# Performance work log

Hardware: AMD Instinct MI355X
Metric: run time of the kernel (lower is better)

Reference implementation:

```python
import jax, jax.numpy as jnp
import numpy as np

B, TQ, TK, D, H = 8, 1024, 1024, 1024, 16
HD = D // H
EPS = 1e-5


def layernorm(x, g, b):
    mu = jnp.mean(x, axis=-1, keepdims=True)
    var = jnp.mean(jnp.square(x - mu), axis=-1, keepdims=True)
    return (x - mu) * jax.lax.rsqrt(var + EPS) * g + b


def setup_inputs() -> dict:
    key = jax.random.key(0)
    ks = jax.random.split(key, 16)
    s = 1.0 / np.sqrt(D)
    return {
        "base": jax.random.normal(ks[0], (B, TQ, D), jnp.float32),
        "fusion": jax.random.normal(ks[1], (B, TK, D), jnp.float32),
        "Wq": jax.random.normal(ks[2], (D, D), jnp.float32) * s,
        "Wk": jax.random.normal(ks[3], (D, D), jnp.float32) * s,
        "Wv": jax.random.normal(ks[4], (D, D), jnp.float32) * s,
        "Wo": jax.random.normal(ks[5], (D, D), jnp.float32) * s,
        "g1": jnp.ones((D,), jnp.float32),
        "b1": jnp.zeros((D,), jnp.float32),
        "g2": jnp.ones((D,), jnp.float32),
        "b2": jnp.zeros((D,), jnp.float32),
        "fc1_w": jax.random.normal(ks[6], (D, D), jnp.float32) * s,
        "fc1_b": jnp.zeros((D,), jnp.float32),
        "fc2_w": jax.random.normal(ks[7], (D, D), jnp.float32) * s,
        "fc2_b": jnp.zeros((D,), jnp.float32),
        "rw": jax.random.normal(ks[8], (D, D), jnp.float32) * s,
        "rb": jnp.zeros((D,), jnp.float32),
        "alpha": jnp.asarray(0.1, jnp.float32),
    }


def reference(base, fusion, Wq, Wk, Wv, Wo, g1, b1, g2, b2,
              fc1_w, fc1_b, fc2_w, fc2_b, rw, rb, alpha):
    def split_heads(x):  # [B,T,D] -> [B,H,T,hd]
        return x.reshape(B, -1, H, HD).transpose(0, 2, 1, 3)

    Q = split_heads(base @ Wq.T)
    K = split_heads(fusion @ Wk.T)
    V = split_heads(fusion @ Wv.T)

    scores = jnp.einsum("bhqd,bhkd->bhqk", Q, K) / jnp.sqrt(jnp.float32(HD))
    attn = jax.nn.softmax(scores, axis=-1)
    # threshold mask (the torch scatter_ with arange indices is an identity copy)
    masked = attn * (attn >= alpha).astype(attn.dtype)
    # second softmax over masked weights (zeros contribute exp(0)=1, as in the original)
    attn2 = jax.nn.softmax(masked, axis=-1)
    out = jnp.einsum("bhqk,bhkd->bhqd", attn2, V)
    out = out.transpose(0, 2, 1, 3).reshape(B, TQ, D)
    out = out @ Wo.T
    x = layernorm(base + out, g1, b1)  # dropout is eval-mode identity
    ff = jax.nn.silu(jax.nn.silu(x @ fc1_w.T + fc1_b) @ fc2_w.T + fc2_b)
    y = layernorm(x + ff, g2, b2)
    final = y @ rw.T + rb
    return final, masked
```

## Files before the change

kernel.cpp:

```cpp
#include <hip/hip_runtime.h>


typedef unsigned short u16;
typedef __attribute__((ext_vector_type(8))) short  bf16x8;
typedef __attribute__((ext_vector_type(4))) short  s16x4;
typedef __attribute__((ext_vector_type(4))) float  f32x4;

#define GLL16(gp, lp) __builtin_amdgcn_global_load_lds(                     \
    (__attribute__((address_space(1))) const void*)(gp),                    \
    (__attribute__((address_space(3))) void*)(lp), 16, 0, 0)

__device__ __forceinline__ u16 f2bf(float x) {
  union { float f; unsigned u; } v; v.f = x;
  return (u16)((v.u + 0x7FFF + ((v.u >> 16) & 1)) >> 16);
}
__device__ __forceinline__ float bf2f(u16 h) {
  union { unsigned u; float f; } v; v.u = ((unsigned)h) << 16;
  return v.f;
}
__device__ __forceinline__ f32x4 zero4() { f32x4 z = {0.f, 0.f, 0.f, 0.f}; return z; }

__global__ __launch_bounds__(256) void pack_act(const float* __restrict__ a,
                                                const float* __restrict__ b,
                                                u16* __restrict__ outa,
                                                u16* __restrict__ outb) {
  size_t i = (size_t)blockIdx.x * 256 + threadIdx.x;
  const f32x4* in = (const f32x4*)(blockIdx.y ? b : a);
  s16x4* out = (s16x4*)(blockIdx.y ? outb : outa);
  f32x4 v = in[i];
  s16x4 o;
  o[0] = (short)f2bf(v[0]); o[1] = (short)f2bf(v[1]);
  o[2] = (short)f2bf(v[2]); o[3] = (short)f2bf(v[3]);
  out[i] = o;
}

__global__ __launch_bounds__(256) void pack_w(
    const float* __restrict__ w0, const float* __restrict__ w1,
    const float* __restrict__ w2, const float* __restrict__ w3,
    const float* __restrict__ w4, const float* __restrict__ w5,
    const float* __restrict__ w6, u16* __restrict__ out) {
  size_t i = (size_t)blockIdx.x * 256 + threadIdx.x;
  const float* in;
  switch (blockIdx.y) {
    case 0: in = w0; break;  case 1: in = w1; break;
    case 2: in = w2; break;  case 3: in = w3; break;
    case 4: in = w4; break;  case 5: in = w5; break;
    default: in = w6; break;
  }
  f32x4 v = ((const f32x4*)in)[i];
  s16x4 o;
  o[0] = (short)f2bf(v[0]); o[1] = (short)f2bf(v[1]);
  o[2] = (short)f2bf(v[2]); o[3] = (short)f2bf(v[3]);
  ((s16x4*)(out + (size_t)blockIdx.y * 1048576))[i] = o;
}

#define EPI_QKV       0
#define EPI_BF16      1
#define EPI_SILU_BF16 4
#define EPI_BIAS_F32  6

template <int EPI>
__global__ __launch_bounds__(256) void gemm_bt(
    const u16* __restrict__ A, int lda,
    const u16* __restrict__ W, int ldw,
    int M, int N, int K,
    float* __restrict__ outF, u16* __restrict__ outU,
    const float* __restrict__ bias,
    const u16* __restrict__ A2) {
  __shared__ u16 As[2][128 * 32];
  __shared__ u16 Bs[2][128 * 32];
  int tid = threadIdx.x;
  int l = tid & 63, w = tid >> 6;
  int wr = w >> 1, wc = w & 1, lr = l & 15, lq = l >> 4;

  int fid = blockIdx.y * 8 + blockIdx.x;
  int swz = (fid & 7) * 64 + (fid >> 3);
  int m0 = (swz >> 3) * 128, n0 = (swz & 7) * 128;

  const u16* Ap = A;
  const u16* Wp = W;
  u16* outUp = outU;
  if constexpr (EPI == EPI_QKV) {
    int z = blockIdx.z;
    if (z) Ap = A2;
    Wp = W + (size_t)z * 1048576;
    outUp = outU + (size_t)z * 8388608;
  }

  f32x4 acc[4][4];
#pragma unroll
  for (int i = 0; i < 4; i++)
#pragma unroll
    for (int j = 0; j < 4; j++) acc[i][j] = zero4();

  auto stage = [&](const u16* src, int ld, int r0, int k0, u16* lds) {
#pragma unroll
    for (int j = 0; j < 2; ++j) {
      int seg = j * 256 + tid;
      int row = seg >> 2, sp = seg & 3;
      const u16* g = src + (size_t)(r0 + row) * ld + k0 +
                     ((sp ^ ((row >> 1) & 3)) << 3);
      GLL16(g, lds + seg * 8);
    }
  };

  int nk = K >> 5;
  stage(Ap, lda, m0, 0, As[0]);
  stage(Wp, ldw, n0, 0, Bs[0]);
  for (int kt = 0; kt < nk; ++kt) {
    __syncthreads();
    if (kt + 1 < nk) {
      stage(Ap, lda, m0, (kt + 1) << 5, As[(kt + 1) & 1]);
      stage(Wp, ldw, n0, (kt + 1) << 5, Bs[(kt + 1) & 1]);
    }
    const u16* Ab = As[kt & 1];
    const u16* Bb = Bs[kt & 1];
    bf16x8 af[4], bw[4];
    int slot = (lq ^ ((lr >> 1) & 3)) << 3;
#pragma unroll
    for (int mi = 0; mi < 4; mi++)
      af[mi] = *(const bf16x8*)&Ab[(wr * 64 + mi * 16 + lr) * 32 + slot];
#pragma unroll
    for (int ni = 0; ni < 4; ni++)
      bw[ni] = *(const bf16x8*)&Bb[(wc * 64 + ni * 16 + lr) * 32 + slot];
#pragma unroll
    for (int mi = 0; mi < 4; mi++)
#pragma unroll
      for (int ni = 0; ni < 4; ni++)
        acc[mi][ni] = __builtin_amdgcn_mfma_f32_16x16x32_bf16(af[mi], bw[ni],
                                                              acc[mi][ni], 0, 0, 0);
  }

#pragma unroll
  for (int mi = 0; mi < 4; mi++) {
#pragma unroll
    for (int ni = 0; ni < 4; ni++) {
      int col = n0 + wc * 64 + ni * 16 + lr;
#pragma unroll
      for (int r = 0; r < 4; r++) {
        int row = m0 + wr * 64 + mi * 16 + lq * 4 + r;
        float v = acc[mi][ni][r];
        if constexpr (EPI == EPI_QKV) {
          int b = row >> 10, t = row & 1023, h = col >> 6, d = col & 63;
          int z = blockIdx.z;
          if (z == 0) {
            outUp[((size_t)(b * 16 + h) * 1024 + t) * 64 + d] = f2bf(v);
          } else if (z == 1) {
            size_t base = ((size_t)(b * 16 + h) * 1024 + t) * 64;
            outUp[base + (((d >> 3) ^ (t & 7)) << 3) + (d & 7)] = f2bf(v);
          } else {
            size_t o = ((size_t)(b * 16 + h) * 64 + d) * 1024 + (t & ~63) +
                       ((((t >> 3) & 7) ^ (d & 7)) << 3) + (t & 7);
            outUp[o] = f2bf(v);
          }
        } else if constexpr (EPI == EPI_BF16) {
          outUp[(size_t)row * N + col] = f2bf(v);
        } else if constexpr (EPI == EPI_SILU_BF16) {
          float z = v + bias[col];
          outUp[(size_t)row * N + col] = f2bf(z / (1.f + __expf(-z)));
        } else {
          outF[(size_t)row * N + col] = v + bias[col];
        }
      }
    }
  }
}

template <int EPI>
__global__ __launch_bounds__(512) void gemm_bt8(
    const u16* __restrict__ A, int lda,
    const u16* __restrict__ W, int ldw,
    int M, int N, int K,
    float* __restrict__ outF, u16* __restrict__ outU,
    const float* __restrict__ bias) {
  __shared__ u16 As[2][128 * 64];
  __shared__ u16 Bs[2][128 * 64];
  int tid = threadIdx.x;
  int l = tid & 63, w = tid >> 6;
  int wr = w >> 2, wc = w & 3, lr = l & 15, lq = l >> 4;

  int fid = blockIdx.y * 8 + blockIdx.x;
  int swz = (fid & 7) * 64 + (fid >> 3);
  int m0 = (swz >> 3) * 128, n0 = (swz & 7) * 128;

  f32x4 acc[4][2];
#pragma unroll
  for (int i = 0; i < 4; i++)
#pragma unroll
    for (int j = 0; j < 2; j++) acc[i][j] = zero4();

  auto stage = [&](const u16* src, int ld, int r0, int k0, u16* lds) {
#pragma unroll
    for (int j = 0; j < 2; ++j) {
      int seg = j * 512 + tid;
      int row = seg >> 3, sp = seg & 7;
      const u16* g = src + (size_t)(r0 + row) * ld + k0 +
                     ((sp ^ (row & 7)) << 3);
      GLL16(g, lds + seg * 8);
    }
  };

  int nk = K >> 6;
  stage(A, lda, m0, 0, As[0]);
  stage(W, ldw, n0, 0, Bs[0]);
  for (int kt = 0; kt < nk; ++kt) {
    __syncthreads();
    if (kt + 1 < nk) {
      stage(A, lda, m0, (kt + 1) << 6, As[(kt + 1) & 1]);
      stage(W, ldw, n0, (kt + 1) << 6, Bs[(kt + 1) & 1]);
    }
    const u16* Ab = As[kt & 1];
    const u16* Bb = Bs[kt & 1];
    bf16x8 af[4][2], bw[2][2];
#pragma unroll
    for (int kk = 0; kk < 2; kk++) {
      int slot = ((kk * 4 + lq) ^ (lr & 7)) << 3;
#pragma unroll
      for (int mi = 0; mi < 4; mi++)
        af[mi][kk] = *(const bf16x8*)&Ab[(wr * 64 + mi * 16 + lr) * 64 + slot];
#pragma unroll
      for (int ni = 0; ni < 2; ni++)
        bw[ni][kk] = *(const bf16x8*)&Bb[(wc * 32 + ni * 16 + lr) * 64 + slot];
    }
#pragma unroll
    for (int kk = 0; kk < 2; kk++)
#pragma unroll
      for (int mi = 0; mi < 4; mi++)
#pragma unroll
        for (int ni = 0; ni < 2; ni++)
          acc[mi][ni] = __builtin_amdgcn_mfma_f32_16x16x32_bf16(
              af[mi][kk], bw[ni][kk], acc[mi][ni], 0, 0, 0);
  }

#pragma unroll
  for (int mi = 0; mi < 4; mi++) {
#pragma unroll
    for (int ni = 0; ni < 2; ni++) {
      int col = n0 + wc * 32 + ni * 16 + lr;
#pragma unroll
      for (int r = 0; r < 4; r++) {
        int row = m0 + wr * 64 + mi * 16 + lq * 4 + r;
        float v = acc[mi][ni][r];
        if constexpr (EPI == EPI_BF16) {
          outU[(size_t)row * N + col] = f2bf(v);
        } else if constexpr (EPI == EPI_SILU_BF16) {
          float z = v + bias[col];
          outU[(size_t)row * N + col] = f2bf(z / (1.f + __expf(-z)));
        } else {
          outF[(size_t)row * N + col] = v + bias[col];
        }
      }
    }
  }
}

__global__ __launch_bounds__(512) void attn_kernel(
    const u16* __restrict__ Q2, const u16* __restrict__ K2,
    const u16* __restrict__ Vt, const float* __restrict__ alphap,
    float* __restrict__ masked_out, u16* __restrict__ attn_out) {
  __shared__ __align__(16) u16 Ks[2][4096];
  __shared__ __align__(16) u16 Vs[2][4096];
  __shared__ __align__(16) u16 Ps[8][16 * 72];

  int tid = threadIdx.x;
  int l = tid & 63, w = tid >> 6, lr = l & 15, lq = l >> 4;

  int bid = blockIdx.x;
  int qi  = bid >> 7;
  int bh  = (bid & 7) * 16 + ((bid >> 3) & 15);
  int h = bh & 15, b = bh >> 4;
  int q0 = qi * 128;

  const u16* Qb = Q2 + (size_t)bh * 1024 * 64;
  const u16* Kb = K2 + (size_t)bh * 1024 * 64;
  const u16* Vb = Vt + (size_t)bh * 64 * 1024;
  float alpha = alphap[0];
  int qw = q0 + w * 16;

  auto stageK = [&](int kc, u16* dst) {
    int seg = tid;
    GLL16(Kb + (size_t)kc * 4096 + seg * 8, dst + seg * 8);
  };
  auto stageV = [&](int kc, u16* dst) {
    int seg = tid;
    GLL16(Vb + (size_t)(seg >> 3) * 1024 + kc * 64 + (seg & 7) * 8, dst + seg * 8);
  };

  bf16x8 qf[2];
#pragma unroll
  for (int kt = 0; kt < 2; kt++)
    qf[kt] = *(const bf16x8*)(Qb + (size_t)(qw + lr) * 64 + kt * 32 + lq * 8);

  float s1[4] = {0.f, 0.f, 0.f, 0.f};

  stageK(0, Ks[0]);
  for (int kc = 0; kc < 16; ++kc) {
    __syncthreads();
    if (kc + 1 < 16) stageK(kc + 1, Ks[(kc + 1) & 1]);
    const u16* Kc = Ks[kc & 1];
    f32x4 acc[4];
#pragma unroll
    for (int ni = 0; ni < 4; ni++) acc[ni] = zero4();
    __builtin_amdgcn_s_setprio(1);
#pragma unroll
    for (int ni = 0; ni < 4; ++ni) {
      int t = ni * 16 + lr;
      bf16x8 k0 = *(const bf16x8*)&Kc[t * 64 + (((0 + lq) ^ (lr & 7)) << 3)];
      bf16x8 k1 = *(const bf16x8*)&Kc[t * 64 + (((4 + lq) ^ (lr & 7)) << 3)];
      acc[ni] = __builtin_amdgcn_mfma_f32_16x16x32_bf16(qf[0], k0, acc[ni], 0, 0, 0);
      acc[ni] = __builtin_amdgcn_mfma_f32_16x16x32_bf16(qf[1], k1, acc[ni], 0, 0, 0);
    }
    __builtin_amdgcn_s_setprio(0);
#pragma unroll
    for (int ni = 0; ni < 4; ni++)
#pragma unroll
      for (int r = 0; r < 4; r++)
        s1[r] += __expf(acc[ni][r] * 0.125f);
  }
#pragma unroll
  for (int r = 0; r < 4; r++) {
    float v = s1[r];
    v += __shfl_xor(v, 1); v += __shfl_xor(v, 2);
    v += __shfl_xor(v, 4); v += __shfl_xor(v, 8);
    s1[r] = 1.0f / v;
  }

  float s2[4] = {0.f, 0.f, 0.f, 0.f};
  f32x4 oacc[4];
#pragma unroll
  for (int dg = 0; dg < 4; dg++) oacc[dg] = zero4();

  stageK(0, Ks[0]);
  stageV(0, Vs[0]);
  for (int kc = 0; kc < 16; ++kc) {
    if (kc == 0) {
      asm volatile("s_waitcnt vmcnt(0) lgkmcnt(0)" ::: "memory");
    } else {
      asm volatile("s_waitcnt vmcnt(16) lgkmcnt(0)" ::: "memory");
    }
    __builtin_amdgcn_s_barrier();
    __builtin_amdgcn_sched_barrier(0);
    if (kc + 1 < 16) {
      stageK(kc + 1, Ks[(kc + 1) & 1]);
      stageV(kc + 1, Vs[(kc + 1) & 1]);
    }
    const u16* Kc = Ks[kc & 1];
    const u16* Vc = Vs[kc & 1];

    f32x4 acc[4];
#pragma unroll
    for (int ni = 0; ni < 4; ni++) acc[ni] = zero4();
    __builtin_amdgcn_s_setprio(1);
#pragma unroll
    for (int ni = 0; ni < 4; ++ni) {
      int t = ni * 16 + lr;
      bf16x8 k0 = *(const bf16x8*)&Kc[t * 64 + (((0 + lq) ^ (lr & 7)) << 3)];
      bf16x8 k1 = *(const bf16x8*)&Kc[t * 64 + (((4 + lq) ^ (lr & 7)) << 3)];
      acc[ni] = __builtin_amdgcn_mfma_f32_16x16x32_bf16(qf[0], k0, acc[ni], 0, 0, 0);
      acc[ni] = __builtin_amdgcn_mfma_f32_16x16x32_bf16(qf[1], k1, acc[ni], 0, 0, 0);
    }
    __builtin_amdgcn_s_setprio(0);

#pragma unroll
    for (int ni = 0; ni < 4; ni++) {
#pragma unroll
      for (int r = 0; r < 4; r++) {
        float e = __expf(acc[ni][r] * 0.125f);
        float a = e * s1[r];
        a = (a >= alpha) ? a : 0.0f;
        size_t row = (size_t)bh * 1024 + qw + lq * 4 + r;
        masked_out[row * 1024 + kc * 64 + ni * 16 + lr] = a;
        float p = __expf(a);
        s2[r] += p;
        Ps[w][(lq * 4 + r) * 72 + ni * 16 + lr] = f2bf(p);
      }
    }
    asm volatile("s_waitcnt lgkmcnt(0)" ::: "memory");

    bf16x8 pf[2];
#pragma unroll
    for (int kt = 0; kt < 2; kt++)
      pf[kt] = *(const bf16x8*)&Ps[w][lr * 72 + kt * 32 + lq * 8];
    __builtin_amdgcn_s_setprio(1);
#pragma unroll
    for (int dg = 0; dg < 4; dg++) {
      int d = dg * 16 + lr;
      bf16x8 v0 = *(const bf16x8*)&Vc[d * 64 + (((0 + lq) ^ (lr & 7)) << 3)];
      bf16x8 v1 = *(const bf16x8*)&Vc[d * 64 + (((4 + lq) ^ (lr & 7)) << 3)];
      oacc[dg] = __builtin_amdgcn_mfma_f32_16x16x32_bf16(pf[0], v0, oacc[dg], 0, 0, 0);
      oacc[dg] = __builtin_amdgcn_mfma_f32_16x16x32_bf16(pf[1], v1, oacc[dg], 0, 0, 0);
    }
    __builtin_amdgcn_s_setprio(0);
  }

#pragma unroll
  for (int r = 0; r < 4; r++) {
    float v = s2[r];
    v += __shfl_xor(v, 1); v += __shfl_xor(v, 2);
    v += __shfl_xor(v, 4); v += __shfl_xor(v, 8);
    s2[r] = 1.0f / v;
  }
#pragma unroll
  for (int dg = 0; dg < 4; dg++)
#pragma unroll
    for (int r = 0; r < 4; r++) {
      int q = qw + lq * 4 + r;
      attn_out[(size_t)(b * 1024 + q) * 1024 + h * 64 + dg * 16 + lr] =
          f2bf(oacc[dg][r] * s2[r]);
    }
}

__global__ __launch_bounds__(256) void ln_kernel(
    const float* __restrict__ A, const u16* __restrict__ Bv,
    const float* __restrict__ g, const float* __restrict__ beta,
    float* __restrict__ outF, u16* __restrict__ outB) {
  __shared__ float red[4];
  int row = blockIdx.x, t = threadIdx.x;
  const float* pa = A + (size_t)row * 1024;
  const u16* pb = Bv + (size_t)row * 1024;
  float v[4];
  float s = 0.f;
#pragma unroll
  for (int i = 0; i < 4; i++) {
    int c = t + 256 * i;
    v[i] = pa[c] + bf2f(pb[c]);
    s += v[i];
  }
#pragma unroll
  for (int off = 1; off < 64; off <<= 1) s += __shfl_xor(s, off);
  if ((t & 63) == 0) red[t >> 6] = s;
  __syncthreads();
  s = red[0] + red[1] + red[2] + red[3];
  float mu = s * 0.0009765625f;
  float q = 0.f;
#pragma unroll
  for (int i = 0; i < 4; i++) { float d = v[i] - mu; q += d * d; }
  __syncthreads();
#pragma unroll
  for (int off = 1; off < 64; off <<= 1) q += __shfl_xor(q, off);
  if ((t & 63) == 0) red[t >> 6] = q;
  __syncthreads();
  q = red[0] + red[1] + red[2] + red[3];
  float rs = rsqrtf(q * 0.0009765625f + 1e-5f);
#pragma unroll
  for (int i = 0; i < 4; i++) {
    int c = t + 256 * i;
    float y = (v[i] - mu) * rs * g[c] + beta[c];
    if (outF) outF[(size_t)row * 1024 + c] = y;
    if (outB) outB[(size_t)row * 1024 + c] = f2bf(y);
  }
}

#define WS_BASEB   0
#define WS_FUSB    16777216
#define WS_W       33554432
#define WS_QKV     48234496
#define WS_ATTNO   98566144
#define WS_X       115343360
#define WS_OB      WS_FUSB
#define WS_XB      WS_BASEB
#define WS_H1      WS_ATTNO
#define WS_FFB     WS_QKV
#define WS_YB      (WS_QKV + 16777216)

extern "C" void kernel_launch(void* const* d_in, const int* in_sizes, int n_in,
                              void* d_out, int out_size, void* d_ws, size_t ws_size,
                              hipStream_t stream) {
  const float* base   = (const float*)d_in[0];
  const float* fusion = (const float*)d_in[1];
  const float* Wq     = (const float*)d_in[2];
  const float* Wk     = (const float*)d_in[3];
  const float* Wv     = (const float*)d_in[4];
  const float* Wo     = (const float*)d_in[5];
  const float* g1     = (const float*)d_in[6];
  const float* b1     = (const float*)d_in[7];
  const float* g2     = (const float*)d_in[8];
  const float* b2     = (const float*)d_in[9];
  const float* fc1w   = (const float*)d_in[10];
  const float* fc1b   = (const float*)d_in[11];
  const float* fc2w   = (const float*)d_in[12];
  const float* fc2b   = (const float*)d_in[13];
  const float* rw     = (const float*)d_in[14];
  const float* rb     = (const float*)d_in[15];
  const float* alphap = (const float*)d_in[16];

  char* ws = (char*)d_ws;
  u16* baseb  = (u16*)(ws + WS_BASEB);
  u16* fusb   = (u16*)(ws + WS_FUSB);
  u16* wall   = (u16*)(ws + WS_W);
  u16* Q2     = (u16*)(ws + WS_QKV);
  u16* attno  = (u16*)(ws + WS_ATTNO);
  u16* obufb  = (u16*)(ws + WS_OB);
  float* x    = (float*)(ws + WS_X);
  u16* xb     = (u16*)(ws + WS_XB);
  u16* h1     = (u16*)(ws + WS_H1);
  u16* ffb    = (u16*)(ws + WS_FFB);
  u16* yb     = (u16*)(ws + WS_YB);

  float* final_out  = (float*)d_out;
  float* masked_out = final_out + 8388608;

  pack_act<<<dim3(8192, 2), 256, 0, stream>>>(base, fusion, baseb, fusb);
  pack_w<<<dim3(1024, 7), 256, 0, stream>>>(Wq, Wk, Wv, Wo, fc1w, fc2w, rw, wall);

  dim3 gg(8, 64);

  gemm_bt<EPI_QKV><<<dim3(8, 64, 3), 256, 0, stream>>>(
      baseb, 1024, wall, 1024, 8192, 1024, 1024, nullptr, Q2, nullptr, fusb);

  attn_kernel<<<dim3(1024), 512, 0, stream>>>(
      Q2, Q2 + 8388608, Q2 + 16777216, alphap, masked_out, attno);

  gemm_bt8<EPI_BF16><<<gg, 512, 0, stream>>>(attno, 1024, wall + 3 * 1048576, 1024,
                                             8192, 1024, 1024, nullptr, obufb, nullptr);
  ln_kernel<<<8192, 256, 0, stream>>>(base, obufb, g1, b1, x, xb);

  gemm_bt8<EPI_SILU_BF16><<<gg, 512, 0, stream>>>(xb, 1024, wall + 4 * 1048576, 1024,
                                                  8192, 1024, 1024, nullptr, h1, fc1b);
  gemm_bt8<EPI_SILU_BF16><<<gg, 512, 0, stream>>>(h1, 1024, wall + 5 * 1048576, 1024,
                                                  8192, 1024, 1024, nullptr, ffb, fc2b);
  ln_kernel<<<8192, 256, 0, stream>>>(x, ffb, g2, b2, nullptr, yb);

  gemm_bt8<EPI_BIAS_F32><<<gg, 512, 0, stream>>>(yb, 1024, wall + 6 * 1048576, 1024,
                                                 8192, 1024, 1024, final_out, nullptr, rb);
}
```

Measured before the change: 939.8 us.

## Replace 128x128 GEMM with 256x128 triple-buffered two-phase pipelined GEMM

The four 8192x1024x1024 GEMMs after attention now use a new kernel with a 256x128 output tile per block, triple-buffered LDS and prefetch two k-steps ahead. Each k-step is split into two phases so that half of the next tile's loads are issued between the MFMA groups, with explicit vmcnt/lgkmcnt waits, barriers and raised wave priority around the MFMA blocks. The aim is more reuse per loaded tile and better overlap of global-to-LDS copies with matrix math. In exchange it needs more LDS (about 144KB) and more accumulator registers, which lowers occupancy, and it hardcodes K=1024 and the grid shape.

```diff
diff --git a/kernel.cpp b/kernel.cpp
--- a/kernel.cpp
+++ b/kernel.cpp
@@ -167,61 +167,81 @@
 }
 
 template <int EPI>
-__global__ __launch_bounds__(512) void gemm_bt8(
-    const u16* __restrict__ A, int lda,
-    const u16* __restrict__ W, int ldw,
-    int M, int N, int K,
-    float* __restrict__ outF, u16* __restrict__ outU,
+__global__ __launch_bounds__(512) void gemm8ph(
+    const u16* __restrict__ A, const u16* __restrict__ W,
+    int N, float* __restrict__ outF, u16* __restrict__ outU,
     const float* __restrict__ bias) {
-  __shared__ u16 As[2][128 * 64];
-  __shared__ u16 Bs[2][128 * 64];
+  __shared__ u16 As[3][256 * 64];
+  __shared__ u16 Bs[3][128 * 64];
   int tid = threadIdx.x;
   int l = tid & 63, w = tid >> 6;
   int wr = w >> 2, wc = w & 3, lr = l & 15, lq = l >> 4;
 
   int fid = blockIdx.y * 8 + blockIdx.x;
-  int swz = (fid & 7) * 64 + (fid >> 3);
-  int m0 = (swz >> 3) * 128, n0 = (swz & 7) * 128;
-
-  f32x4 acc[4][2];
-#pragma unroll
-  for (int i = 0; i < 4; i++)
+  int swz = (fid & 7) * 32 + (fid >> 3);
+  int m0 = (swz >> 3) * 256, n0 = (swz & 7) * 128;
+
+  f32x4 acc[8][2];
+#pragma unroll
+  for (int i = 0; i < 8; i++)
 #pragma unroll
     for (int j = 0; j < 2; j++) acc[i][j] = zero4();
 
-  auto stage = [&](const u16* src, int ld, int r0, int k0, u16* lds) {
+  auto stageA = [&](int kt, int h, u16* lds) {
 #pragma unroll
     for (int j = 0; j < 2; ++j) {
       int seg = j * 512 + tid;
       int row = seg >> 3, sp = seg & 7;
-      const u16* g = src + (size_t)(r0 + row) * ld + k0 +
+      const u16* g = A + (size_t)(m0 + h * 128 + row) * 1024 + (kt << 6) +
                      ((sp ^ (row & 7)) << 3);
-      GLL16(g, lds + seg * 8);
+      GLL16(g, lds + h * 8192 + seg * 8);
     }
   };
-
-  int nk = K >> 6;
-  stage(A, lda, m0, 0, As[0]);
-  stage(W, ldw, n0, 0, Bs[0]);
-  for (int kt = 0; kt < nk; ++kt) {
-    __syncthreads();
-    if (kt + 1 < nk) {
-      stage(A, lda, m0, (kt + 1) << 6, As[(kt + 1) & 1]);
-      stage(W, ldw, n0, (kt + 1) << 6, Bs[(kt + 1) & 1]);
-    }
-    const u16* Ab = As[kt & 1];
-    const u16* Bb = Bs[kt & 1];
+  auto stageB = [&](int kt, int h, u16* lds) {
+    int seg = tid;
+    int row = seg >> 3, sp = seg & 7;
+    const u16* g = W + (size_t)(n0 + h * 64 + row) * 1024 + (kt << 6) +
+                   ((sp ^ (row & 7)) << 3);
+    GLL16(g, lds + h * 4096 + seg * 8);
+  };
+
+  stageA(0, 0, As[0]); stageB(0, 0, Bs[0]);
+  stageA(0, 1, As[0]); stageB(0, 1, Bs[0]);
+  stageA(1, 0, As[1]); stageB(1, 0, Bs[1]);
+  stageA(1, 1, As[1]); stageB(1, 1, Bs[1]);
+
+  for (int kt = 0; kt < 16; ++kt) {
+    const u16* Ab = As[kt % 3];
+    const u16* Bb = Bs[kt % 3];
+    if (kt == 15) {
+      asm volatile("s_waitcnt vmcnt(0)" ::: "memory");
+    } else {
+      asm volatile("s_waitcnt vmcnt(6)" ::: "memory");
+    }
+    __builtin_amdgcn_s_barrier();
+
     bf16x8 af[4][2], bw[2][2];
 #pragma unroll
     for (int kk = 0; kk < 2; kk++) {
-      int slot = ((kk * 4 + lq) ^ (lr & 7)) << 3;
-#pragma unroll
-      for (int mi = 0; mi < 4; mi++)
-        af[mi][kk] = *(const bf16x8*)&Ab[(wr * 64 + mi * 16 + lr) * 64 + slot];
-#pragma unroll
-      for (int ni = 0; ni < 2; ni++)
-        bw[ni][kk] = *(const bf16x8*)&Bb[(wc * 32 + ni * 16 + lr) * 64 + slot];
-    }
+#pragma unroll
+      for (int mi = 0; mi < 4; mi++) {
+        int r = wr * 128 + mi * 16 + lr;
+        af[mi][kk] = *(const bf16x8*)&Ab[r * 64 + (((kk * 4 + lq) ^ (r & 7)) << 3)];
+      }
+#pragma unroll
+      for (int ni = 0; ni < 2; ni++) {
+        int r = wc * 32 + ni * 16 + lr;
+        bw[ni][kk] = *(const bf16x8*)&Bb[r * 64 + (((kk * 4 + lq) ^ (r & 7)) << 3)];
+      }
+    }
+    if (kt + 2 < 16) {
+      stageA(kt + 2, 0, As[(kt + 2) % 3]);
+      stageB(kt + 2, 0, Bs[(kt + 2) % 3]);
+    }
+    __builtin_amdgcn_s_barrier();
+    asm volatile("s_waitcnt lgkmcnt(0)" ::: "memory");
+    __builtin_amdgcn_sched_barrier(0);
+    __builtin_amdgcn_s_setprio(1);
 #pragma unroll
     for (int kk = 0; kk < 2; kk++)
 #pragma unroll
@@ -230,16 +250,44 @@
         for (int ni = 0; ni < 2; ni++)
           acc[mi][ni] = __builtin_amdgcn_mfma_f32_16x16x32_bf16(
               af[mi][kk], bw[ni][kk], acc[mi][ni], 0, 0, 0);
-  }
-
-#pragma unroll
-  for (int mi = 0; mi < 4; mi++) {
+    __builtin_amdgcn_s_setprio(0);
+    __builtin_amdgcn_s_barrier();
+
+    bf16x8 ag[4][2];
+#pragma unroll
+    for (int kk = 0; kk < 2; kk++)
+#pragma unroll
+      for (int mi = 0; mi < 4; mi++) {
+        int r = wr * 128 + (mi + 4) * 16 + lr;
+        ag[mi][kk] = *(const bf16x8*)&Ab[r * 64 + (((kk * 4 + lq) ^ (r & 7)) << 3)];
+      }
+    if (kt + 2 < 16) {
+      stageA(kt + 2, 1, As[(kt + 2) % 3]);
+      stageB(kt + 2, 1, Bs[(kt + 2) % 3]);
+    }
+    __builtin_amdgcn_s_barrier();
+    asm volatile("s_waitcnt lgkmcnt(0)" ::: "memory");
+    __builtin_amdgcn_sched_barrier(0);
+    __builtin_amdgcn_s_setprio(1);
+#pragma unroll
+    for (int kk = 0; kk < 2; kk++)
+#pragma unroll
+      for (int mi = 0; mi < 4; mi++)
+#pragma unroll
+        for (int ni = 0; ni < 2; ni++)
+          acc[mi + 4][ni] = __builtin_amdgcn_mfma_f32_16x16x32_bf16(
+              ag[mi][kk], bw[ni][kk], acc[mi + 4][ni], 0, 0, 0);
+    __builtin_amdgcn_s_setprio(0);
+  }
+
+#pragma unroll
+  for (int mi = 0; mi < 8; mi++) {
 #pragma unroll
     for (int ni = 0; ni < 2; ni++) {
       int col = n0 + wc * 32 + ni * 16 + lr;
 #pragma unroll
       for (int r = 0; r < 4; r++) {
-        int row = m0 + wr * 64 + mi * 16 + lq * 4 + r;
+        int row = m0 + wr * 128 + mi * 16 + lq * 4 + r;
         float v = acc[mi][ni][r];
         if constexpr (EPI == EPI_BF16) {
           outU[(size_t)row * N + col] = f2bf(v);
@@ -503,24 +551,24 @@
   pack_act<<<dim3(8192, 2), 256, 0, stream>>>(base, fusion, baseb, fusb);
   pack_w<<<dim3(1024, 7), 256, 0, stream>>>(Wq, Wk, Wv, Wo, fc1w, fc2w, rw, wall);
 
-  dim3 gg(8, 64);
-
   gemm_bt<EPI_QKV><<<dim3(8, 64, 3), 256, 0, stream>>>(
       baseb, 1024, wall, 1024, 8192, 1024, 1024, nullptr, Q2, nullptr, fusb);
 
   attn_kernel<<<dim3(1024), 512, 0, stream>>>(
       Q2, Q2 + 8388608, Q2 + 16777216, alphap, masked_out, attno);
 
-  gemm_bt8<EPI_BF16><<<gg, 512, 0, stream>>>(attno, 1024, wall + 3 * 1048576, 1024,
-                                             8192, 1024, 1024, nullptr, obufb, nullptr);
+  dim3 g8(8, 32);
+
+  gemm8ph<EPI_BF16><<<g8, 512, 0, stream>>>(attno, wall + 3 * 1048576,
+                                            1024, nullptr, obufb, nullptr);
   ln_kernel<<<8192, 256, 0, stream>>>(base, obufb, g1, b1, x, xb);
 
-  gemm_bt8<EPI_SILU_BF16><<<gg, 512, 0, stream>>>(xb, 1024, wall + 4 * 1048576, 1024,
-                                                  8192, 1024, 1024, nullptr, h1, fc1b);
-  gemm_bt8<EPI_SILU_BF16><<<gg, 512, 0, stream>>>(h1, 1024, wall + 5 * 1048576, 1024,
-                                                  8192, 1024, 1024, nullptr, ffb, fc2b);
+  gemm8ph<EPI_SILU_BF16><<<g8, 512, 0, stream>>>(xb, wall + 4 * 1048576,
+                                                 1024, nullptr, h1, fc1b);
+  gemm8ph<EPI_SILU_BF16><<<g8, 512, 0, stream>>>(h1, wall + 5 * 1048576,
+                                                 1024, nullptr, ffb, fc2b);
   ln_kernel<<<8192, 256, 0, stream>>>(x, ffb, g2, b2, nullptr, yb);
 
-  gemm_bt8<EPI_BIAS_F32><<<gg, 512, 0, stream>>>(yb, 1024, wall + 6 * 1048576, 1024,
-                                                 8192, 1024, 1024, final_out, nullptr, rb);
-}
+  gemm8ph<EPI_BIAS_F32><<<g8, 512, 0, stream>>>(yb, wall + 6 * 1048576,
+                                                1024, final_out, nullptr, rb);
+}
```

Measured after the change: 947.8 us. About the same (+0.9%).

## Decompose second softmax into a V row-sum plus a sparse correction and skip empty tiles

Applied to the files above, without the earlier changes.

Rewrites the second softmax as a sum over keys of (1 + (exp(a)-1)) times V. The all-ones part becomes a per-head V row-sum, computed once into shared memory, and the normaliser becomes 1024 plus the sum of the corrections. The P·V MFMA stage now runs only when some element in the wave's tile survives the alpha threshold, so the per-chunk exp, LDS writes and matrix multiplies are skipped for empty tiles. V staging into LDS is removed: V fragments are read straight from global memory when needed, which drops half the staging traffic. The cost is uncached global reads whenever a tile does have kept values, plus slightly different bf16 rounding in the P·V path.

```diff
diff --git a/kernel.cpp b/kernel.cpp
--- a/kernel.cpp
+++ b/kernel.cpp
@@ -259,8 +259,8 @@
     const u16* __restrict__ Vt, const float* __restrict__ alphap,
     float* __restrict__ masked_out, u16* __restrict__ attn_out) {
   __shared__ __align__(16) u16 Ks[2][4096];
-  __shared__ __align__(16) u16 Vs[2][4096];
   __shared__ __align__(16) u16 Ps[8][16 * 72];
+  __shared__ float vsumf[64];
 
   int tid = threadIdx.x;
   int l = tid & 63, w = tid >> 6, lr = l & 15, lq = l >> 4;
@@ -271,20 +271,28 @@
   int h = bh & 15, b = bh >> 4;
   int q0 = qi * 128;
 
-  const u16* Qb = Q2 + (size_t)bh * 1024 * 64;
-  const u16* Kb = K2 + (size_t)bh * 1024 * 64;
-  const u16* Vb = Vt + (size_t)bh * 64 * 1024;
+  const u16* Qb = Q2 + (size_t)bh * 65536;
+  const u16* Kb = K2 + (size_t)bh * 65536;
+  const u16* Vb = Vt + (size_t)bh * 65536;
   float alpha = alphap[0];
   int qw = q0 + w * 16;
 
   auto stageK = [&](int kc, u16* dst) {
-    int seg = tid;
-    GLL16(Kb + (size_t)kc * 4096 + seg * 8, dst + seg * 8);
+    GLL16(Kb + (size_t)kc * 4096 + tid * 8, dst + tid * 8);
   };
-  auto stageV = [&](int kc, u16* dst) {
-    int seg = tid;
-    GLL16(Vb + (size_t)(seg >> 3) * 1024 + kc * 64 + (seg & 7) * 8, dst + seg * 8);
-  };
+
+  {
+    const u16* vrow = Vb + (size_t)(tid >> 3) * 1024 + (size_t)(tid & 7) * 128;
+    float vs = 0.f;
+#pragma unroll
+    for (int i = 0; i < 16; i++) {
+      bf16x8 vv = *(const bf16x8*)&vrow[i * 8];
+#pragma unroll
+      for (int j = 0; j < 8; j++) vs += bf2f((u16)vv[j]);
+    }
+    vs += __shfl_xor(vs, 1); vs += __shfl_xor(vs, 2); vs += __shfl_xor(vs, 4);
+    if ((tid & 7) == 0) vsumf[tid >> 3] = vs;
+  }
 
   bf16x8 qf[2];
 #pragma unroll
@@ -331,7 +339,6 @@
   for (int dg = 0; dg < 4; dg++) oacc[dg] = zero4();
 
   stageK(0, Ks[0]);
-  stageV(0, Vs[0]);
   for (int kc = 0; kc < 16; ++kc) {
     if (kc == 0) {
       asm volatile("s_waitcnt vmcnt(0) lgkmcnt(0)" ::: "memory");
@@ -340,12 +347,8 @@
     }
     __builtin_amdgcn_s_barrier();
     __builtin_amdgcn_sched_barrier(0);
-    if (kc + 1 < 16) {
-      stageK(kc + 1, Ks[(kc + 1) & 1]);
-      stageV(kc + 1, Vs[(kc + 1) & 1]);
-    }
+    if (kc + 1 < 16) stageK(kc + 1, Ks[(kc + 1) & 1]);
     const u16* Kc = Ks[kc & 1];
-    const u16* Vc = Vs[kc & 1];
 
     f32x4 acc[4];
 #pragma unroll
@@ -361,6 +364,8 @@
     }
     __builtin_amdgcn_s_setprio(0);
 
+    float aval[4][4];
+    int kept = 0;
 #pragma unroll
     for (int ni = 0; ni < 4; ni++) {
 #pragma unroll
@@ -368,29 +373,42 @@
         float e = __expf(acc[ni][r] * 0.125f);
         float a = e * s1[r];
         a = (a >= alpha) ? a : 0.0f;
+        aval[ni][r] = a;
+        kept |= (a != 0.0f);
         size_t row = (size_t)bh * 1024 + qw + lq * 4 + r;
         masked_out[row * 1024 + kc * 64 + ni * 16 + lr] = a;
-        float p = __expf(a);
-        s2[r] += p;
-        Ps[w][(lq * 4 + r) * 72 + ni * 16 + lr] = f2bf(p);
       }
     }
-    asm volatile("s_waitcnt lgkmcnt(0)" ::: "memory");
-
-    bf16x8 pf[2];
-#pragma unroll
-    for (int kt = 0; kt < 2; kt++)
-      pf[kt] = *(const bf16x8*)&Ps[w][lr * 72 + kt * 32 + lq * 8];
-    __builtin_amdgcn_s_setprio(1);
-#pragma unroll
-    for (int dg = 0; dg < 4; dg++) {
-      int d = dg * 16 + lr;
-      bf16x8 v0 = *(const bf16x8*)&Vc[d * 64 + (((0 + lq) ^ (lr & 7)) << 3)];
-      bf16x8 v1 = *(const bf16x8*)&Vc[d * 64 + (((4 + lq) ^ (lr & 7)) << 3)];
-      oacc[dg] = __builtin_amdgcn_mfma_f32_16x16x32_bf16(pf[0], v0, oacc[dg], 0, 0, 0);
-      oacc[dg] = __builtin_amdgcn_mfma_f32_16x16x32_bf16(pf[1], v1, oacc[dg], 0, 0, 0);
-    }
-    __builtin_amdgcn_s_setprio(0);
+
+    if (__any(kept)) {
+#pragma unroll
+      for (int ni = 0; ni < 4; ni++) {
+#pragma unroll
+        for (int r = 0; r < 4; r++) {
+          float a = aval[ni][r];
+          float pm1 = (a != 0.0f) ? (__expf(a) - 1.0f) : 0.0f;
+          s2[r] += pm1;
+          Ps[w][(lq * 4 + r) * 72 + ni * 16 + lr] = f2bf(pm1);
+        }
+      }
+      asm volatile("s_waitcnt lgkmcnt(0)" ::: "memory");
+      bf16x8 pf[2];
+#pragma unroll
+      for (int kt = 0; kt < 2; kt++)
+        pf[kt] = *(const bf16x8*)&Ps[w][lr * 72 + kt * 32 + lq * 8];
+      __builtin_amdgcn_s_setprio(1);
+#pragma unroll
+      for (int dg = 0; dg < 4; dg++) {
+        int d = dg * 16 + lr;
+        bf16x8 v0 = *(const bf16x8*)&Vb[(size_t)d * 1024 + kc * 64 +
+                                        (((0 + lq) ^ (d & 7)) << 3)];
+        bf16x8 v1 = *(const bf16x8*)&Vb[(size_t)d * 1024 + kc * 64 +
+                                        (((4 + lq) ^ (d & 7)) << 3)];
+        oacc[dg] = __builtin_amdgcn_mfma_f32_16x16x32_bf16(pf[0], v0, oacc[dg], 0, 0, 0);
+        oacc[dg] = __builtin_amdgcn_mfma_f32_16x16x32_bf16(pf[1], v1, oacc[dg], 0, 0, 0);
+      }
+      __builtin_amdgcn_s_setprio(0);
+    }
   }
 
 #pragma unroll
@@ -398,7 +416,7 @@
     float v = s2[r];
     v += __shfl_xor(v, 1); v += __shfl_xor(v, 2);
     v += __shfl_xor(v, 4); v += __shfl_xor(v, 8);
-    s2[r] = 1.0f / v;
+    s2[r] = 1.0f / (1024.0f + v);
   }
 #pragma unroll
   for (int dg = 0; dg < 4; dg++)
@@ -406,7 +424,7 @@
     for (int r = 0; r < 4; r++) {
       int q = qw + lq * 4 + r;
       attn_out[(size_t)(b * 1024 + q) * 1024 + h * 64 + dg * 16 + lr] =
-          f2bf(oacc[dg][r] * s2[r]);
+          f2bf((vsumf[dg * 16 + lr] + oacc[dg][r]) * s2[r]);
     }
 }
 
@@ -503,13 +521,13 @@
   pack_act<<<dim3(8192, 2), 256, 0, stream>>>(base, fusion, baseb, fusb);
   pack_w<<<dim3(1024, 7), 256, 0, stream>>>(Wq, Wk, Wv, Wo, fc1w, fc2w, rw, wall);
 
-  dim3 gg(8, 64);
-
   gemm_bt<EPI_QKV><<<dim3(8, 64, 3), 256, 0, stream>>>(
       baseb, 1024, wall, 1024, 8192, 1024, 1024, nullptr, Q2, nullptr, fusb);
 
   attn_kernel<<<dim3(1024), 512, 0, stream>>>(
       Q2, Q2 + 8388608, Q2 + 16777216, alphap, masked_out, attno);
+
+  dim3 gg(8, 64);
 
   gemm_bt8<EPI_BF16><<<gg, 512, 0, stream>>>(attno, 1024, wall + 3 * 1048576, 1024,
                                              8192, 1024, 1024, nullptr, obufb, nullptr);
```

Measured after the change: 916.9 us. -2.4%, faster.
